# Optimization experiments

Hardware: AMD Instinct MI355X
Metric: run time of the kernel (lower is better)

The kernel has to match this reference:

```python
import jax, jax.numpy as jnp
import numpy as np
import math

B, L, C = 16, 4096, 512
SPARSE_RATIO = 0.6
NUM_KEEP = math.ceil(L * SPARSE_RATIO)  # 2458


def setup_inputs() -> dict:
    key = jax.random.key(0)
    k1, k2, k3 = jax.random.split(key, 3)
    return {
        "tokens": jax.random.normal(k1, (B, L, C), dtype=jnp.float32),
        "attention_x": jax.random.normal(k2, (B, L), dtype=jnp.float32),
        "attention_y": jax.random.normal(k3, (B, L), dtype=jnp.float32),
    }


def reference(tokens, attention_x, attention_y):
    eps = 1e-6
    # coverage-fused score: alpha = sigmoid(1 - mean(ay)/mean(ax))
    coverage = attention_y.mean(axis=1) / (attention_x.mean(axis=1) + eps)  # [B]
    alpha = jax.nn.sigmoid(1.0 - coverage)                                  # [B]
    beta = 1.0 - alpha
    score = alpha[:, None] * attention_x + beta[:, None] * attention_y      # [B, L]

    # full descending sort of scores
    order = jnp.argsort(-score, axis=1)                                     # [B, L]
    score_sort = jnp.take_along_axis(score, order, axis=1)                  # [B, L]

    keep_policy = order[:, :NUM_KEEP]                                       # [B, K]
    non_keep_policy = order[:, NUM_KEEP:]                                   # [B, L-K]

    # scatter 1s at kept positions
    batch_idx = jnp.arange(B)[:, None]
    score_mask = jnp.zeros_like(score).at[batch_idx, keep_policy].set(1.0)  # [B, L]

    # gather kept / pruned tokens
    select_tokens = jnp.take_along_axis(tokens, keep_policy[:, :, None], axis=1)      # [B, K, C]
    non_tokens = jnp.take_along_axis(tokens, non_keep_policy[:, :, None], axis=1)     # [B, L-K, C]

    # softmax-weighted merge of pruned tokens into one extra token
    non_keep_score = jax.nn.softmax(score_sort[:, NUM_KEEP:], axis=1)[:, :, None]     # [B, L-K, 1]
    extra_token = jnp.sum(non_tokens * non_keep_score, axis=1, keepdims=True)         # [B, 1, C]

    return select_tokens, extra_token, score_mask
```

## Files before the change

### kernel.cpp

```cpp
#include <hip/hip_runtime.h>
#include <math.h>

#define NB 16
#define NL 4096
#define NC 512
#define NC4 128
#define NKEEP 2458
#define KEEPB 76
#define NTAILB 52

typedef float f32x4 __attribute__((ext_vector_type(4)));


__global__ void __launch_bounds__(1024) k_front(const float* __restrict__ ax,
                                                const float* __restrict__ ay,
                                                unsigned long long* __restrict__ key,
                                                int* __restrict__ rank,
                                                float* __restrict__ alpha,
                                                float* __restrict__ beta,
                                                unsigned* __restrict__ smaxu) {
  int b = blockIdx.x;
  int tid = threadIdx.x;
  __shared__ float s_ab[2];
  __shared__ unsigned redmaxu[16];
  if (tid < 64) {
    int lane = tid;
    float sx = 0.0f, sy = 0.0f;
    if (lane < 32) {
      const float* px = ax + b * NL + lane * 128;
      const float* py = ay + b * NL + lane * 128;
      float r[8], q[8];
#pragma unroll
      for (int j = 0; j < 8; ++j) { r[j] = px[j]; q[j] = py[j]; }
      for (int i = 8; i < 128; i += 8) {
#pragma unroll
        for (int j = 0; j < 8; ++j) {
          r[j] = __fadd_rn(r[j], px[i + j]);
          q[j] = __fadd_rn(q[j], py[i + j]);
        }
      }
      sx = __fadd_rn(__fadd_rn(__fadd_rn(r[0], r[1]), __fadd_rn(r[2], r[3])),
                     __fadd_rn(__fadd_rn(r[4], r[5]), __fadd_rn(r[6], r[7])));
      sy = __fadd_rn(__fadd_rn(__fadd_rn(q[0], q[1]), __fadd_rn(q[2], q[3])),
                     __fadd_rn(__fadd_rn(q[4], q[5]), __fadd_rn(q[6], q[7])));
    }
#pragma unroll
    for (int m = 1; m <= 16; m <<= 1) {
      sx = __fadd_rn(sx, __shfl_xor(sx, m, 64));
      sy = __fadd_rn(sy, __shfl_xor(sy, m, 64));
    }
    if (lane == 0) {
      float mx = __fdiv_rn(sx, 4096.0f);
      float my = __fdiv_rn(sy, 4096.0f);
      float cov = __fdiv_rn(my, __fadd_rn(mx, 1e-6f));
      float z = __fsub_rn(1.0f, cov);
      double a = 1.0 / (1.0 + exp(-(double)z));
      float af = (float)a;
      alpha[b] = af;
      beta[b] = __fsub_rn(1.0f, af);
      s_ab[0] = af;
      s_ab[1] = __fsub_rn(1.0f, af);
    }
  }
  __syncthreads();
  float af = s_ab[0], bf = s_ab[1];
  unsigned m = 0;
#pragma unroll
  for (int p = 0; p < 4; ++p) {
    int l = p * 1024 + tid;
    int idx = b * NL + l;
    float s = __fadd_rn(__fmul_rn(af, ax[idx]), __fmul_rn(bf, ay[idx]));
    unsigned u = __float_as_uint(s);
    unsigned su = u ^ ((u & 0x80000000u) ? 0xFFFFFFFFu : 0x80000000u);
    key[idx] = ((unsigned long long)(~su) << 32) | (unsigned)l;
    rank[idx] = 0;
    m = (su > m) ? su : m;
  }
#pragma unroll
  for (int d = 1; d < 64; d <<= 1) {
    unsigned o = (unsigned)__shfl_xor((int)m, d, 64);
    m = (o > m) ? o : m;
  }
  if ((tid & 63) == 0) redmaxu[tid >> 6] = m;
  __syncthreads();
  if (tid == 0) {
    unsigned M = redmaxu[0];
#pragma unroll
    for (int k = 1; k < 16; ++k) M = (redmaxu[k] > M) ? redmaxu[k] : M;
    smaxu[b] = M;
  }
}

__global__ void __launch_bounds__(256) k_rank(const unsigned long long* __restrict__ key,
                                              int* __restrict__ rank) {
  __shared__ unsigned long long tile[512];
  int b = blockIdx.z;
  int tid = threadIdx.x;
  const unsigned long long* kb = key + b * NL;
  int ibase = blockIdx.x * 1024;
  unsigned long long ki[4];
#pragma unroll
  for (int k = 0; k < 4; ++k) ki[k] = kb[ibase + k * 256 + tid];
  int j0 = blockIdx.y * 512;
  tile[tid] = kb[j0 + tid];
  tile[tid + 256] = kb[j0 + 256 + tid];
  __syncthreads();
  const ulonglong2* t2 = (const ulonglong2*)tile;
  int cnt[4] = {0, 0, 0, 0};
#pragma unroll 8
  for (int jj = 0; jj < 256; ++jj) {
    ulonglong2 p = t2[jj];
#pragma unroll
    for (int k = 0; k < 4; ++k) {
      cnt[k] += (p.x < ki[k]) ? 1 : 0;
      cnt[k] += (p.y < ki[k]) ? 1 : 0;
    }
  }
#pragma unroll
  for (int k = 0; k < 4; ++k)
    atomicAdd(&rank[b * NL + ibase + k * 256 + tid], cnt[k]);
}

__global__ void __launch_bounds__(256) k_mid(const float* __restrict__ ax,
                                             const float* __restrict__ ay,
                                             const float* __restrict__ alpha,
                                             const float* __restrict__ beta,
                                             const int* __restrict__ rank,
                                             const unsigned* __restrict__ smaxu,
                                             float* __restrict__ w,
                                             float* __restrict__ mask_out,
                                             int* __restrict__ order,
                                             float* __restrict__ Zpart) {
  int gid = blockIdx.x * 256 + threadIdx.x;
  int b = gid >> 12;
  int l = gid & (NL - 1);
  int r = rank[gid];
  float s = __fadd_rn(__fmul_rn(alpha[b], ax[gid]), __fmul_rn(beta[b], ay[gid]));
  mask_out[gid] = (r < NKEEP) ? 1.0f : 0.0f;
  unsigned SU = smaxu[b];
  float smax = (SU & 0x80000000u) ? __uint_as_float(SU ^ 0x80000000u)
                                  : __uint_as_float(~SU);
  float wi = (r >= NKEEP) ? expf(s - smax) : 0.0f;
  w[gid] = wi;
  order[b * NL + r] = l;
  float zs = wi;
#pragma unroll
  for (int d = 1; d < 64; d <<= 1) zs += __shfl_xor(zs, d, 64);
  __shared__ float zred[4];
  if ((threadIdx.x & 63) == 0) zred[threadIdx.x >> 6] = zs;
  __syncthreads();
  if (threadIdx.x == 0)
    Zpart[blockIdx.x] = (zred[0] + zred[1]) + (zred[2] + zred[3]);
}

__global__ void __launch_bounds__(256) k_perm(const f32x4* __restrict__ tok,
                                              const int* __restrict__ order,
                                              const float* __restrict__ w,
                                              f32x4* __restrict__ sel,
                                              f32x4* __restrict__ partial) {
  int b = blockIdx.y;
  int bx = blockIdx.x;
  int p0 = bx * 32;
  int tid = threadIdx.x;
  int col = tid & 127;
  int g = tid >> 7;
  __shared__ int ssrc[32];
  __shared__ float swt[32];
  __shared__ float accsh[512];
  if (tid < 32) {
    int p = p0 + tid;
    int src = order[b * NL + p];
    ssrc[tid] = src;
    swt[tid] = w[b * NL + src];
  }
  __syncthreads();

  const f32x4* tb = tok + (size_t)b * NL * NC4 + col;
  f32x4 v[16];
#pragma unroll
  for (int k = 0; k < 16; ++k)
    v[k] = tb[(size_t)ssrc[g * 16 + k] * NC4];

  f32x4* sb = sel + (size_t)b * NKEEP * NC4 + col;
  float a0 = 0.f, a1 = 0.f, a2 = 0.f, a3 = 0.f;
#pragma unroll
  for (int k = 0; k < 16; ++k) {
    int p = p0 + g * 16 + k;
    if (p < NKEEP) {
      sb[(size_t)p * NC4] = v[k];
    } else {
      float wk = swt[g * 16 + k];
      a0 = fmaf(wk, v[k].x, a0);
      a1 = fmaf(wk, v[k].y, a1);
      a2 = fmaf(wk, v[k].z, a2);
      a3 = fmaf(wk, v[k].w, a3);
    }
  }

  if (bx >= KEEPB) {
    if (g == 1) {
      accsh[col * 4 + 0] = a0; accsh[col * 4 + 1] = a1;
      accsh[col * 4 + 2] = a2; accsh[col * 4 + 3] = a3;
    }
    __syncthreads();
    if (g == 0) {
      f32x4 o;
      o.x = a0 + accsh[col * 4 + 0];
      o.y = a1 + accsh[col * 4 + 1];
      o.z = a2 + accsh[col * 4 + 2];
      o.w = a3 + accsh[col * 4 + 3];
      partial[(size_t)(b * NTAILB + (bx - KEEPB)) * 128 + col] = o;
    }
  }
}

__global__ void __launch_bounds__(512) k_back(const float* __restrict__ partial,
                                              const float* __restrict__ Zpart,
                                              float* __restrict__ extra) {
  int b = blockIdx.x;
  int c = threadIdx.x;
  float Zb = 0.0f;
#pragma unroll
  for (int k = 0; k < 16; ++k) Zb += Zpart[b * 16 + k];
  const float* p = partial + (size_t)b * NTAILB * 512 + c;
  float a0 = 0.f, a1 = 0.f, a2 = 0.f, a3 = 0.f;
#pragma unroll
  for (int j = 0; j < NTAILB; j += 4) {
    a0 += p[(size_t)(j + 0) * 512];
    a1 += p[(size_t)(j + 1) * 512];
    a2 += p[(size_t)(j + 2) * 512];
    a3 += p[(size_t)(j + 3) * 512];
  }
  extra[b * NC + c] = ((a0 + a1) + (a2 + a3)) / Zb;
}

extern "C" void kernel_launch(void* const* d_in, const int* in_sizes, int n_in,
                              void* d_out, int out_size, void* d_ws, size_t ws_size,
                              hipStream_t stream) {
  (void)in_sizes; (void)n_in; (void)out_size; (void)ws_size;
  const f32x4* tok = (const f32x4*)d_in[0];
  const float* ax = (const float*)d_in[1];
  const float* ay = (const float*)d_in[2];

  unsigned long long* key = (unsigned long long*)d_ws;
  int* rank = (int*)((char*)d_ws + 524288);
  float* w = (float*)((char*)d_ws + 786432);
  int* order = (int*)((char*)d_ws + 1048576);
  f32x4* partial = (f32x4*)((char*)d_ws + 1310720);
  float* scalars = (float*)((char*)d_ws + 3145728);
  float* alpha = scalars;
  float* beta = scalars + 16;
  unsigned* smaxu = (unsigned*)(scalars + 32);
  float* Zpart = scalars + 48;

  float* out = (float*)d_out;
  f32x4* sel = (f32x4*)out;
  float* extra = out + (size_t)NB * NKEEP * NC;
  float* mask = extra + (size_t)NB * NC;

  k_front<<<NB, 1024, 0, stream>>>(ax, ay, key, rank, alpha, beta, smaxu);
  k_rank<<<dim3(4, 8, NB), 256, 0, stream>>>(key, rank);
  k_mid<<<256, 256, 0, stream>>>(ax, ay, alpha, beta, rank, smaxu, w, mask, order, Zpart);
  k_perm<<<dim3(128, NB), 256, 0, stream>>>(tok, order, w, sel, partial);
  k_back<<<NB, 512, 0, stream>>>((const float*)partial, Zpart, extra);
}
```

Before: 67.76 us.

## Replace all-pairs rank counting with chunk bitonic sort plus binary search ranking

Replaces the O(L^2) all-pairs comparison kernel with atomics by a per-512-chunk bitonic sort in shared memory. Each element's rank then comes from binary searches into the eight sorted chunks inside k_mid, which now uses 1024-thread blocks holding a whole batch's sorted keys in LDS. This removes the rank zeroing and the atomics, but adds many __syncthreads in the bitonic network and a 32KB LDS load per k_mid block, and k_mid runs with fewer blocks (64).

```diff
diff --git a/kernel.cpp b/kernel.cpp
--- a/kernel.cpp
+++ b/kernel.cpp
@@ -15,7 +15,6 @@
 __global__ void __launch_bounds__(1024) k_front(const float* __restrict__ ax,
                                                 const float* __restrict__ ay,
                                                 unsigned long long* __restrict__ key,
-                                                int* __restrict__ rank,
                                                 float* __restrict__ alpha,
                                                 float* __restrict__ beta,
                                                 unsigned* __restrict__ smaxu) {
@@ -73,7 +72,6 @@
     unsigned u = __float_as_uint(s);
     unsigned su = u ^ ((u & 0x80000000u) ? 0xFFFFFFFFu : 0x80000000u);
     key[idx] = ((unsigned long long)(~su) << 32) | (unsigned)l;
-    rank[idx] = 0;
     m = (su > m) ? su : m;
   }
 #pragma unroll
@@ -91,51 +89,77 @@
   }
 }
 
-__global__ void __launch_bounds__(256) k_rank(const unsigned long long* __restrict__ key,
-                                              int* __restrict__ rank) {
-  __shared__ unsigned long long tile[512];
-  int b = blockIdx.z;
-  int tid = threadIdx.x;
-  const unsigned long long* kb = key + b * NL;
-  int ibase = blockIdx.x * 1024;
-  unsigned long long ki[4];
-#pragma unroll
-  for (int k = 0; k < 4; ++k) ki[k] = kb[ibase + k * 256 + tid];
-  int j0 = blockIdx.y * 512;
-  tile[tid] = kb[j0 + tid];
-  tile[tid + 256] = kb[j0 + 256 + tid];
-  __syncthreads();
-  const ulonglong2* t2 = (const ulonglong2*)tile;
-  int cnt[4] = {0, 0, 0, 0};
-#pragma unroll 8
-  for (int jj = 0; jj < 256; ++jj) {
-    ulonglong2 p = t2[jj];
-#pragma unroll
-    for (int k = 0; k < 4; ++k) {
-      cnt[k] += (p.x < ki[k]) ? 1 : 0;
-      cnt[k] += (p.y < ki[k]) ? 1 : 0;
-    }
-  }
-#pragma unroll
-  for (int k = 0; k < 4; ++k)
-    atomicAdd(&rank[b * NL + ibase + k * 256 + tid], cnt[k]);
-}
-
-__global__ void __launch_bounds__(256) k_mid(const float* __restrict__ ax,
-                                             const float* __restrict__ ay,
-                                             const float* __restrict__ alpha,
-                                             const float* __restrict__ beta,
-                                             const int* __restrict__ rank,
-                                             const unsigned* __restrict__ smaxu,
-                                             float* __restrict__ w,
-                                             float* __restrict__ mask_out,
-                                             int* __restrict__ order,
-                                             float* __restrict__ Zpart) {
-  int gid = blockIdx.x * 256 + threadIdx.x;
-  int b = gid >> 12;
-  int l = gid & (NL - 1);
-  int r = rank[gid];
+__global__ void __launch_bounds__(256) k_sort(const unsigned long long* __restrict__ key,
+                                              unsigned long long* __restrict__ skey) {
+  __shared__ unsigned long long lk[512];
+  int b = blockIdx.y;
+  int c = blockIdx.x;
+  int t = threadIdx.x;
+  const unsigned long long* kb = key + (size_t)b * NL + c * 512;
+  lk[t] = kb[t];
+  lk[t + 256] = kb[t + 256];
+  __syncthreads();
+  for (int k = 2; k <= 512; k <<= 1) {
+    for (int j = k >> 1; j > 0; j >>= 1) {
+#pragma unroll
+      for (int e = 0; e < 2; ++e) {
+        int i = t + e * 256;
+        int l = i ^ j;
+        if (l > i) {
+          unsigned long long a = lk[i], bb = lk[l];
+          bool up = ((i & k) == 0);
+          if ((a > bb) == up) { lk[i] = bb; lk[l] = a; }
+        }
+      }
+      __syncthreads();
+    }
+  }
+  unsigned long long* sb = skey + ((size_t)b * 8 + c) * 512;
+  sb[t] = lk[t];
+  sb[t + 256] = lk[t + 256];
+}
+
+__global__ void __launch_bounds__(1024) k_mid(const float* __restrict__ ax,
+                                              const float* __restrict__ ay,
+                                              const float* __restrict__ alpha,
+                                              const float* __restrict__ beta,
+                                              const unsigned long long* __restrict__ skey,
+                                              const unsigned* __restrict__ smaxu,
+                                              float* __restrict__ w,
+                                              float* __restrict__ mask_out,
+                                              int* __restrict__ order,
+                                              float* __restrict__ Zpart) {
+  __shared__ unsigned long long lsk[4096];
+  __shared__ float zred[16];
+  int bx = blockIdx.x;
+  int b = bx >> 2;
+  int q = bx & 3;
+  int t = threadIdx.x;
+  const unsigned long long* sb = skey + (size_t)b * NL;
+#pragma unroll
+  for (int k = 0; k < 4; ++k) lsk[k * 1024 + t] = sb[k * 1024 + t];
+  __syncthreads();
+
+  int l = q * 1024 + t;
+  int gid = b * NL + l;
   float s = __fadd_rn(__fmul_rn(alpha[b], ax[gid]), __fmul_rn(beta[b], ay[gid]));
+  unsigned u = __float_as_uint(s);
+  unsigned su = u ^ ((u & 0x80000000u) ? 0xFFFFFFFFu : 0x80000000u);
+  unsigned long long ki = ((unsigned long long)(~su) << 32) | (unsigned)l;
+
+  int r = 0;
+#pragma unroll
+  for (int c = 0; c < 8; ++c) {
+    const unsigned long long* base = lsk + c * 512;
+    int pos = 0;
+#pragma unroll
+    for (int step = 512; step >= 1; step >>= 1) {
+      int cand = pos + step;
+      if (cand <= 512 && base[cand - 1] < ki) pos = cand;
+    }
+    r += pos;
+  }
+
   mask_out[gid] = (r < NKEEP) ? 1.0f : 0.0f;
   unsigned SU = smaxu[b];
   float smax = (SU & 0x80000000u) ? __uint_as_float(SU ^ 0x80000000u)
@@ -143,14 +167,18 @@
   float wi = (r >= NKEEP) ? expf(s - smax) : 0.0f;
   w[gid] = wi;
   order[b * NL + r] = l;
+
   float zs = wi;
 #pragma unroll
   for (int d = 1; d < 64; d <<= 1) zs += __shfl_xor(zs, d, 64);
-  __shared__ float zred[4];
-  if ((threadIdx.x & 63) == 0) zred[threadIdx.x >> 6] = zs;
-  __syncthreads();
-  if (threadIdx.x == 0)
-    Zpart[blockIdx.x] = (zred[0] + zred[1]) + (zred[2] + zred[3]);
+  if ((t & 63) == 0) zred[t >> 6] = zs;
+  __syncthreads();
+  if (t == 0) {
+    float z = 0.0f;
+#pragma unroll
+    for (int k = 0; k < 16; ++k) z += zred[k];
+    Zpart[bx] = z;
+  }
 }
 
 __global__ void __launch_bounds__(256) k_perm(const f32x4* __restrict__ tok,
@@ -221,7 +249,7 @@
   int c = threadIdx.x;
   float Zb = 0.0f;
 #pragma unroll
-  for (int k = 0; k < 16; ++k) Zb += Zpart[b * 16 + k];
+  for (int k = 0; k < 4; ++k) Zb += Zpart[b * 4 + k];
   const float* p = partial + (size_t)b * NTAILB * 512 + c;
   float a0 = 0.f, a1 = 0.f, a2 = 0.f, a3 = 0.f;
 #pragma unroll
@@ -243,11 +271,11 @@
   const float* ay = (const float*)d_in[2];
 
   unsigned long long* key = (unsigned long long*)d_ws;
-  int* rank = (int*)((char*)d_ws + 524288);
-  float* w = (float*)((char*)d_ws + 786432);
-  int* order = (int*)((char*)d_ws + 1048576);
-  f32x4* partial = (f32x4*)((char*)d_ws + 1310720);
-  float* scalars = (float*)((char*)d_ws + 3145728);
+  unsigned long long* skey = (unsigned long long*)((char*)d_ws + 524288);
+  float* w = (float*)((char*)d_ws + 1048576);
+  int* order = (int*)((char*)d_ws + 1310720);
+  f32x4* partial = (f32x4*)((char*)d_ws + 1572864);
+  float* scalars = (float*)((char*)d_ws + 3407872);
   float* alpha = scalars;
   float* beta = scalars + 16;
   unsigned* smaxu = (unsigned*)(scalars + 32);
@@ -258,9 +286,9 @@
   float* extra = out + (size_t)NB * NKEEP * NC;
   float* mask = extra + (size_t)NB * NC;
 
-  k_front<<<NB, 1024, 0, stream>>>(ax, ay, key, rank, alpha, beta, smaxu);
-  k_rank<<<dim3(4, 8, NB), 256, 0, stream>>>(key, rank);
-  k_mid<<<256, 256, 0, stream>>>(ax, ay, alpha, beta, rank, smaxu, w, mask, order, Zpart);
+  k_front<<<NB, 1024, 0, stream>>>(ax, ay, key, alpha, beta, smaxu);
+  k_sort<<<dim3(8, NB), 256, 0, stream>>>(key, skey);
+  k_mid<<<64, 1024, 0, stream>>>(ax, ay, alpha, beta, skey, smaxu, w, mask, order, Zpart);
   k_perm<<<dim3(128, NB), 256, 0, stream>>>(tok, order, w, sel, partial);
   k_back<<<NB, 512, 0, stream>>>((const float*)partial, Zpart, extra);
 }
```

Result: no change. 67.55 us (-0.3%).

## Replace rank-counting sort with per-batch LDS bitonic sort fused with mid stage

Applied to the files above, without the earlier changes.

Merges the front, rank and mid kernels into one kernel per batch. It builds the 64-bit score/index keys in shared memory, bitonic-sorts them in place, and then emits order, mask, softmax weights and the partition sum directly. This removes the O(L^2) all-pairs rank counting with global atomics, the key/rank round trips through global memory and two launches. In exchange the sort runs on only 16 workgroups and needs many barrier-separated stages, which leaves most compute units idle.

```diff
diff --git a/kernel.cpp b/kernel.cpp
--- a/kernel.cpp
+++ b/kernel.cpp
@@ -12,19 +12,20 @@
 typedef float f32x4 __attribute__((ext_vector_type(4)));
 
 
-__global__ void __launch_bounds__(1024) k_front(const float* __restrict__ ax,
-                                                const float* __restrict__ ay,
-                                                unsigned long long* __restrict__ key,
-                                                int* __restrict__ rank,
-                                                float* __restrict__ alpha,
-                                                float* __restrict__ beta,
-                                                unsigned* __restrict__ smaxu) {
+__global__ void __launch_bounds__(1024) k_sortmid(const float* __restrict__ ax,
+                                                  const float* __restrict__ ay,
+                                                  float* __restrict__ wp,
+                                                  float* __restrict__ mask_out,
+                                                  int* __restrict__ order,
+                                                  float* __restrict__ Zpart) {
+  __shared__ unsigned long long lsk[4096];
+  __shared__ float s_ab[2];
+  __shared__ float zred[16];
   int b = blockIdx.x;
-  int tid = threadIdx.x;
-  __shared__ float s_ab[2];
-  __shared__ unsigned redmaxu[16];
-  if (tid < 64) {
-    int lane = tid;
+  int t = threadIdx.x;
+
+  if (t < 64) {
+    int lane = t;
     float sx = 0.0f, sy = 0.0f;
     if (lane < 32) {
       const float* px = ax + b * NL + lane * 128;
@@ -56,106 +57,73 @@
       float z = __fsub_rn(1.0f, cov);
       double a = 1.0 / (1.0 + exp(-(double)z));
       float af = (float)a;
-      alpha[b] = af;
-      beta[b] = __fsub_rn(1.0f, af);
       s_ab[0] = af;
       s_ab[1] = __fsub_rn(1.0f, af);
     }
   }
   __syncthreads();
   float af = s_ab[0], bf = s_ab[1];
-  unsigned m = 0;
-#pragma unroll
-  for (int p = 0; p < 4; ++p) {
-    int l = p * 1024 + tid;
+
+#pragma unroll
+  for (int e = 0; e < 4; ++e) {
+    int l = e * 1024 + t;
     int idx = b * NL + l;
     float s = __fadd_rn(__fmul_rn(af, ax[idx]), __fmul_rn(bf, ay[idx]));
     unsigned u = __float_as_uint(s);
     unsigned su = u ^ ((u & 0x80000000u) ? 0xFFFFFFFFu : 0x80000000u);
-    key[idx] = ((unsigned long long)(~su) << 32) | (unsigned)l;
-    rank[idx] = 0;
-    m = (su > m) ? su : m;
-  }
-#pragma unroll
-  for (int d = 1; d < 64; d <<= 1) {
-    unsigned o = (unsigned)__shfl_xor((int)m, d, 64);
-    m = (o > m) ? o : m;
-  }
-  if ((tid & 63) == 0) redmaxu[tid >> 6] = m;
-  __syncthreads();
-  if (tid == 0) {
-    unsigned M = redmaxu[0];
-#pragma unroll
-    for (int k = 1; k < 16; ++k) M = (redmaxu[k] > M) ? redmaxu[k] : M;
-    smaxu[b] = M;
-  }
-}
-
-__global__ void __launch_bounds__(256) k_rank(const unsigned long long* __restrict__ key,
-                                              int* __restrict__ rank) {
-  __shared__ unsigned long long tile[512];
-  int b = blockIdx.z;
-  int tid = threadIdx.x;
-  const unsigned long long* kb = key + b * NL;
-  int ibase = blockIdx.x * 1024;
-  unsigned long long ki[4];
-#pragma unroll
-  for (int k = 0; k < 4; ++k) ki[k] = kb[ibase + k * 256 + tid];
-  int j0 = blockIdx.y * 512;
-  tile[tid] = kb[j0 + tid];
-  tile[tid + 256] = kb[j0 + 256 + tid];
-  __syncthreads();
-  const ulonglong2* t2 = (const ulonglong2*)tile;
-  int cnt[4] = {0, 0, 0, 0};
-#pragma unroll 8
-  for (int jj = 0; jj < 256; ++jj) {
-    ulonglong2 p = t2[jj];
-#pragma unroll
-    for (int k = 0; k < 4; ++k) {
-      cnt[k] += (p.x < ki[k]) ? 1 : 0;
-      cnt[k] += (p.y < ki[k]) ? 1 : 0;
-    }
-  }
-#pragma unroll
-  for (int k = 0; k < 4; ++k)
-    atomicAdd(&rank[b * NL + ibase + k * 256 + tid], cnt[k]);
-}
-
-__global__ void __launch_bounds__(256) k_mid(const float* __restrict__ ax,
-                                             const float* __restrict__ ay,
-                                             const float* __restrict__ alpha,
-                                             const float* __restrict__ beta,
-                                             const int* __restrict__ rank,
-                                             const unsigned* __restrict__ smaxu,
-                                             float* __restrict__ w,
-                                             float* __restrict__ mask_out,
-                                             int* __restrict__ order,
-                                             float* __restrict__ Zpart) {
-  int gid = blockIdx.x * 256 + threadIdx.x;
-  int b = gid >> 12;
-  int l = gid & (NL - 1);
-  int r = rank[gid];
-  float s = __fadd_rn(__fmul_rn(alpha[b], ax[gid]), __fmul_rn(beta[b], ay[gid]));
-  mask_out[gid] = (r < NKEEP) ? 1.0f : 0.0f;
-  unsigned SU = smaxu[b];
-  float smax = (SU & 0x80000000u) ? __uint_as_float(SU ^ 0x80000000u)
-                                  : __uint_as_float(~SU);
-  float wi = (r >= NKEEP) ? expf(s - smax) : 0.0f;
-  w[gid] = wi;
-  order[b * NL + r] = l;
-  float zs = wi;
+    lsk[l] = ((unsigned long long)(~su) << 32) | (unsigned)l;
+  }
+  __syncthreads();
+
+  for (int k = 2; k <= 4096; k <<= 1) {
+    for (int j = k >> 1; j > 0; j >>= 1) {
+#pragma unroll
+      for (int e = 0; e < 4; ++e) {
+        int i = e * 1024 + t;
+        int l2 = i ^ j;
+        if (l2 > i) {
+          unsigned long long a = lsk[i], bb = lsk[l2];
+          bool up = ((i & k) == 0);
+          if ((a > bb) == up) { lsk[i] = bb; lsk[l2] = a; }
+        }
+      }
+      __syncthreads();
+    }
+  }
+
+  unsigned su0 = ~(unsigned)(lsk[0] >> 32);
+  float smax = (su0 & 0x80000000u) ? __uint_as_float(su0 ^ 0x80000000u)
+                                   : __uint_as_float(~su0);
+  float zs = 0.0f;
+#pragma unroll
+  for (int e = 0; e < 4; ++e) {
+    int p = e * 1024 + t;
+    unsigned long long kk = lsk[p];
+    int l = (int)(unsigned)kk;
+    unsigned su = ~(unsigned)(kk >> 32);
+    float s = (su & 0x80000000u) ? __uint_as_float(su ^ 0x80000000u)
+                                 : __uint_as_float(~su);
+    order[b * NL + p] = l;
+    float wi = (p >= NKEEP) ? expf(s - smax) : 0.0f;
+    wp[b * NL + p] = wi;
+    mask_out[b * NL + l] = (p < NKEEP) ? 1.0f : 0.0f;
+    zs += wi;
+  }
 #pragma unroll
   for (int d = 1; d < 64; d <<= 1) zs += __shfl_xor(zs, d, 64);
-  __shared__ float zred[4];
-  if ((threadIdx.x & 63) == 0) zred[threadIdx.x >> 6] = zs;
-  __syncthreads();
-  if (threadIdx.x == 0)
-    Zpart[blockIdx.x] = (zred[0] + zred[1]) + (zred[2] + zred[3]);
+  if ((t & 63) == 0) zred[t >> 6] = zs;
+  __syncthreads();
+  if (t == 0) {
+    float z = 0.0f;
+#pragma unroll
+    for (int k = 0; k < 16; ++k) z += zred[k];
+    Zpart[b] = z;
+  }
 }
 
 __global__ void __launch_bounds__(256) k_perm(const f32x4* __restrict__ tok,
                                               const int* __restrict__ order,
-                                              const float* __restrict__ w,
+                                              const float* __restrict__ wp,
                                               f32x4* __restrict__ sel,
                                               f32x4* __restrict__ partial) {
   int b = blockIdx.y;
@@ -169,9 +137,8 @@
   __shared__ float accsh[512];
   if (tid < 32) {
     int p = p0 + tid;
-    int src = order[b * NL + p];
-    ssrc[tid] = src;
-    swt[tid] = w[b * NL + src];
+    ssrc[tid] = order[b * NL + p];
+    swt[tid] = wp[b * NL + p];
   }
   __syncthreads();
 
@@ -219,9 +186,7 @@
                                               float* __restrict__ extra) {
   int b = blockIdx.x;
   int c = threadIdx.x;
-  float Zb = 0.0f;
-#pragma unroll
-  for (int k = 0; k < 16; ++k) Zb += Zpart[b * 16 + k];
+  float Zb = Zpart[b];
   const float* p = partial + (size_t)b * NTAILB * 512 + c;
   float a0 = 0.f, a1 = 0.f, a2 = 0.f, a3 = 0.f;
 #pragma unroll
@@ -242,25 +207,17 @@
   const float* ax = (const float*)d_in[1];
   const float* ay = (const float*)d_in[2];
 
-  unsigned long long* key = (unsigned long long*)d_ws;
-  int* rank = (int*)((char*)d_ws + 524288);
-  float* w = (float*)((char*)d_ws + 786432);
-  int* order = (int*)((char*)d_ws + 1048576);
-  f32x4* partial = (f32x4*)((char*)d_ws + 1310720);
-  float* scalars = (float*)((char*)d_ws + 3145728);
-  float* alpha = scalars;
-  float* beta = scalars + 16;
-  unsigned* smaxu = (unsigned*)(scalars + 32);
-  float* Zpart = scalars + 48;
+  float* wp = (float*)d_ws;
+  int* order = (int*)((char*)d_ws + 262144);
+  f32x4* partial = (f32x4*)((char*)d_ws + 524288);
+  float* Zpart = (float*)((char*)d_ws + 2359296);
 
   float* out = (float*)d_out;
   f32x4* sel = (f32x4*)out;
   float* extra = out + (size_t)NB * NKEEP * NC;
   float* mask = extra + (size_t)NB * NC;
 
-  k_front<<<NB, 1024, 0, stream>>>(ax, ay, key, rank, alpha, beta, smaxu);
-  k_rank<<<dim3(4, 8, NB), 256, 0, stream>>>(key, rank);
-  k_mid<<<256, 256, 0, stream>>>(ax, ay, alpha, beta, rank, smaxu, w, mask, order, Zpart);
-  k_perm<<<dim3(128, NB), 256, 0, stream>>>(tok, order, w, sel, partial);
+  k_sortmid<<<NB, 1024, 0, stream>>>(ax, ay, wp, mask, order, Zpart);
+  k_perm<<<dim3(128, NB), 256, 0, stream>>>(tok, order, wp, sel, partial);
   k_back<<<NB, 512, 0, stream>>>((const float*)partial, Zpart, extra);
 }
```

New measurement: 90.66 us. 1.34x slower.
